# Optimization experiments

Measured on AMD Instinct MI355X. Metric: run time of the kernel, lower is better.

## Reference

```python
import jax, jax.numpy as jnp
import numpy as np

B, K, N, M = 32, 128, 128, 256  # batch, num_classes(==n_dim), n_dim, samples-per-matrix
EPSILON = 0.1
LAMBDA_SOFTMAX = 0.1
LEARNING_RATE = 0.01
BN_EPS = 1e-5


def setup_inputs() -> dict:
    key = jax.random.key(0)
    k1, k2, k3 = jax.random.split(key, 3)
    x = jax.random.normal(k1, (B, N, M), dtype=jnp.float32)
    A = jax.random.normal(k2, (K, N, N), dtype=jnp.float32) * 0.1
    EC_proto = jnp.einsum('kij,klj->kil', A, A)  # per-class PSD prototype covariances (K,N,N)
    EC_count = jax.random.uniform(k3, (K,), dtype=jnp.float32, minval=1.0, maxval=100.0)
    return {"x": x, "EC_proto": EC_proto, "EC_count": EC_count}


def reference(x, EC_proto, EC_count):
    n = x.shape[1]
    dtype = x.dtype
    # BatchNorm1d(num_classes, affine=False, track_running_stats=False): batch stats over (N, L)
    mean = x.mean(axis=(0, 2), keepdims=True)
    var = x.var(axis=(0, 2), keepdims=True)  # biased variance, as torch uses for normalization
    x = (x - mean) / jnp.sqrt(var + BN_EPS)

    eye = jnp.eye(n, dtype=dtype)
    total = EC_count.sum()
    has_counts = total > 1e-6

    # E branch: global expansion operator
    e_alpha = jnp.where(has_counts, n / (EPSILON * EPSILON * total), jnp.zeros((), dtype))
    e = e_alpha * jnp.linalg.inv(e_alpha * EC_proto.sum(0) + eye)  # (N,N)
    e_x_z = jnp.einsum('ij,bjm->bim', e, x)  # (B,N,M)

    # C branch: per-class compression operators
    bool_depth = (EC_count != 0).astype(dtype)  # (K,)
    count_fix = EC_count + (1.0 - bool_depth)
    c_alpha = (n / (count_fix * EPSILON * EPSILON) * bool_depth)[:, None, None]  # (K,1,1)
    c = c_alpha * jnp.linalg.inv(c_alpha * EC_proto + eye[None])  # (K,N,N)
    c_x_z = jnp.einsum('kij,bjm->bkim', c, x)  # (B,K,N,M)

    # Frobenius norm per (b,k), rescaled to sum to 10 over classes
    norm = jnp.sqrt((c_x_z * c_x_z).sum(axis=(2, 3)))  # (B,K)
    norm = 10.0 * norm / norm.sum(axis=1, keepdims=True)

    pi = jax.nn.softmax(-LAMBDA_SOFTMAX * norm, axis=1) * bool_depth  # (B,K)
    gama = jnp.where(has_counts, EC_count / total, jnp.zeros_like(EC_count))  # (K,)

    z_d = e_x_z - jnp.einsum('k,bkim,bk->bim', gama, c_x_z, pi)  # (B,N,M)
    return x + LEARNING_RATE * z_d
```

## Files before the change

### kernel.cpp

```cpp
#include <hip/hip_runtime.h>
#include <math.h>

#define Bb 32
#define Kk 128
#define Nn 128
#define Mm 256
#define EPS2 0.01f
#define LAMBDA_S 0.1f
#define LR 0.01f
#define BN_EPS_C 1e-5f

#define SWZ(c) (((c) & 14) | (((c) & 1) << 4) | (((c) >> 4) & 1))

__device__ __forceinline__ float readlane_f(float v, int lane) {
  return __int_as_float(__builtin_amdgcn_readlane(__float_as_int(v), lane));
}

__global__ void kPre(const float* __restrict__ P, float* __restrict__ Psum) {
  int e = blockIdx.x * 256 + threadIdx.x;
  float s = 0.f;
  #pragma unroll 8
  for (int k = 0; k < Kk; ++k) s += P[(size_t)k * 16384 + e];
  Psum[e] = s;
}

__global__ __launch_bounds__(512, 1) void kIR(
    const float* __restrict__ P, const float* __restrict__ Psum,
    const float* __restrict__ cnt, float* __restrict__ C,
    const float* __restrict__ x, float* __restrict__ R,
    float* __restrict__ rbuf, float* __restrict__ meanB,
    float* __restrict__ rstdB) {
  __shared__ __align__(16) float LB[8448];
  int bx = blockIdx.x;
  int t = threadIdx.x;

  if (bx < 129) {
    float* Mt = LB;
    float* Rb = LB + 2112;
    float* redc = LB + 4160;
    int mat = bx;
    int tx = t & 15;
    int wy = t >> 4;

    float cv = cnt[t & 127];
    float sr = cv;
    #pragma unroll
    for (int o = 32; o > 0; o >>= 1) sr += __shfl_down(sr, o, 64);
    if ((t & 63) == 0) redc[t >> 6] = sr;
    __syncthreads();
    float total = redc[0] + redc[1];
    bool has = total > 1e-6f;
    float av;
    if (mat < 128) {
      float c = cnt[mat];
      float bk = (c != 0.0f) ? 1.0f : 0.0f;
      float cfix = c + (1.0f - bk);
      av = (float)Nn / (cfix * EPS2) * bk;
    } else {
      av = has ? ((float)Nn / (EPS2 * total)) : 0.0f;
    }
    const float* src = (mat < 128) ? (P + (size_t)mat * 16384) : Psum;

    float a[4][8];
    #pragma unroll
    for (int i = 0; i < 4; ++i) {
      int row = wy * 4 + i;
      float4 p0 = *(const float4*)&src[row * 128 + tx * 8];
      float4 p1 = *(const float4*)&src[row * 128 + tx * 8 + 4];
      a[i][0] = av * p0.x; a[i][1] = av * p0.y; a[i][2] = av * p0.z; a[i][3] = av * p0.w;
      a[i][4] = av * p1.x; a[i][5] = av * p1.y; a[i][6] = av * p1.z; a[i][7] = av * p1.w;
      if (tx == (wy >> 1)) a[i][(wy & 1) * 4 + i] += 1.0f;
    }

    for (int kb = 0; kb < 8; ++kb) {
      int k0 = kb * 16;
      if ((wy >> 2) == kb) {
        int d = wy & 3;
        #pragma unroll
        for (int i = 0; i < 4; ++i) {
          *(float4*)&Rb[(d * 4 + i) * 128 + SWZ(2 * tx) * 4] =
              make_float4(a[i][0], a[i][1], a[i][2], a[i][3]);
          *(float4*)&Rb[(d * 4 + i) * 128 + SWZ(2 * tx + 1) * 4] =
              make_float4(a[i][4], a[i][5], a[i][6], a[i][7]);
        }
      }
      if ((tx >> 1) == kb) {
        int dh = tx & 1;
        #pragma unroll
        for (int i = 0; i < 4; ++i)
          #pragma unroll
          for (int j = 0; j < 8; ++j)
            Mt[(dh * 8 + j) * 132 + wy * 4 + i] = a[i][j];
      }
      __syncthreads();

      if (t < 64) {
        int l = t;
        float m[2][16];
        #pragma unroll
        for (int d = 0; d < 2; ++d)
          #pragma unroll
          for (int j = 0; j < 16; ++j)
            m[d][j] = Mt[j * 132 + 2 * l + d];
        #pragma unroll
        for (int q = 0; q < 16; ++q) {
          int lq = (k0 + q) >> 1;
          float pr[16];
          #pragma unroll
          for (int j = 0; j < 16; ++j) pr[j] = readlane_f(m[q & 1][j], lq);
          float piv = pr[q];
          float r0 = __builtin_amdgcn_rcpf(piv);
          float pinv = r0 * (2.0f - piv * r0);
          #pragma unroll
          for (int d = 0; d < 2; ++d) {
            float f = m[d][q];
            bool isp = (2 * l + d == k0 + q);
            float g = isp ? (1.0f - pinv) : f * pinv;
            #pragma unroll
            for (int j = 0; j < 16; ++j) m[d][j] = fmaf(-g, pr[j], m[d][j]);
            m[d][q] = isp ? pinv : -g;
          }
        }
        #pragma unroll
        for (int d = 0; d < 2; ++d)
          #pragma unroll
          for (int j = 0; j < 16; ++j)
            Mt[j * 132 + 2 * l + d] = m[d][j];
      }
      __syncthreads();

      if ((wy >> 2) == kb) {
        #pragma unroll
        for (int i = 0; i < 4; ++i)
          #pragma unroll
          for (int j = 0; j < 8; ++j) a[i][j] = 0.0f;
      }
      #pragma unroll
      for (int q = 0; q < 16; ++q) {
        float4 m0 = *(const float4*)&Mt[q * 132 + wy * 4];
        float4 r0 = *(const float4*)&Rb[q * 128 + SWZ(2 * tx) * 4];
        float4 r1 = *(const float4*)&Rb[q * 128 + SWZ(2 * tx + 1) * 4];
        float mq[4] = {m0.x, m0.y, m0.z, m0.w};
        float rq[8] = {r0.x, r0.y, r0.z, r0.w, r1.x, r1.y, r1.z, r1.w};
        #pragma unroll
        for (int i = 0; i < 4; ++i)
          #pragma unroll
          for (int j = 0; j < 8; ++j)
            a[i][j] = fmaf(mq[i], rq[j], a[i][j]);
      }
      if ((tx >> 1) == kb) {
        int dh = tx & 1;
        #pragma unroll
        for (int j = 0; j < 8; ++j) {
          float4 v0 = *(const float4*)&Mt[(dh * 8 + j) * 132 + wy * 4];
          a[0][j] = v0.x; a[1][j] = v0.y; a[2][j] = v0.z; a[3][j] = v0.w;
        }
      }
      __syncthreads();
    }

    float* dst = C + (size_t)mat * 16384;
    #pragma unroll
    for (int i = 0; i < 4; ++i) {
      int row = wy * 4 + i;
      float4 v0 = make_float4(av * a[i][0], av * a[i][1], av * a[i][2], av * a[i][3]);
      float4 v1 = make_float4(av * a[i][4], av * a[i][5], av * a[i][6], av * a[i][7]);
      *(float4*)&dst[row * 128 + tx * 8] = v0;
      *(float4*)&dst[row * 128 + tx * 8 + 4] = v1;
    }
  } else if (bx < 193) {
    int bxx = bx - 129;
    int b = bxx >> 1;
    int jbase = (bxx & 1) * 64;
    float* X = LB;
    int tx = t & 15, wy = t >> 4;
    float acc[4][4] = {};
    float rsum = 0.f;
    for (int mc = 0; mc < Mm; mc += 64) {
      __syncthreads();
      #pragma unroll
      for (int c = 0; c < 16; ++c) {
        int e = c * 512 + t;
        int i = e >> 6, mm = e & 63;
        X[i * 65 + mm] = x[(size_t)b * (Nn * Mm) + i * Mm + mc + mm];
      }
      __syncthreads();
      if (t < 128) {
        #pragma unroll
        for (int mm = 0; mm < 64; ++mm) rsum += X[t * 65 + mm];
      }
      for (int mm = 0; mm < 64; ++mm) {
        float ai[4], bj[4];
        #pragma unroll
        for (int q = 0; q < 4; ++q) ai[q] = X[(wy * 4 + q) * 65 + mm];
        #pragma unroll
        for (int q = 0; q < 4; ++q) bj[q] = X[(jbase + tx * 4 + q) * 65 + mm];
        #pragma unroll
        for (int qi = 0; qi < 4; ++qi)
          #pragma unroll
          for (int qj = 0; qj < 4; ++qj)
            acc[qi][qj] = fmaf(ai[qi], bj[qj], acc[qi][qj]);
      }
    }
    float* dst = R + (size_t)b * 16384;
    #pragma unroll
    for (int qi = 0; qi < 4; ++qi) {
      float4 v = make_float4(acc[qi][0], acc[qi][1], acc[qi][2], acc[qi][3]);
      *(float4*)&dst[(wy * 4 + qi) * 128 + jbase + tx * 4] = v;
    }
    if (jbase == 0 && t < 128) rbuf[b * 128 + t] = rsum;
  } else {
    int n = bx - 193;
    int m = t & 255, bh = t >> 8;
    float s = 0.f, s2 = 0.f;
    #pragma unroll
    for (int q = 0; q < 16; ++q) {
      float v = x[(size_t)(bh * 16 + q) * (Nn * Mm) + n * Mm + m];
      s += v; s2 += v * v;
    }
    #pragma unroll
    for (int o = 32; o > 0; o >>= 1) {
      s += __shfl_down(s, o, 64);
      s2 += __shfl_down(s2, o, 64);
    }
    if ((t & 63) == 0) { LB[t >> 6] = s; LB[16 + (t >> 6)] = s2; }
    __syncthreads();
    if (t == 0) {
      float S = 0.f, S2 = 0.f;
      #pragma unroll
      for (int w = 0; w < 8; ++w) { S += LB[w]; S2 += LB[16 + w]; }
      float mean = S * (1.0f / (Bb * Mm));
      float var = S2 * (1.0f / (Bb * Mm)) - mean * mean;
      meanB[n] = mean;
      rstdB[n] = 1.0f / sqrtf(var + BN_EPS_C);
    }
  }
}

__global__ __launch_bounds__(256, 1) void kGN(const float* __restrict__ C,
                                              const float* __restrict__ R,
                                              const float* __restrict__ rbuf,
                                              const float* __restrict__ meanB,
                                              const float* __restrict__ rstdB,
                                              float* __restrict__ norm2h) {
  __shared__ __align__(16) float LB[128 * 128];
  __shared__ float redb[4][32];
  __shared__ float muL[128], rsL[128], uL[128];
  int k = blockIdx.x >> 2, qh = blockIdx.x & 3;
  int t = threadIdx.x;
  if (t < 128) { muL[t] = meanB[t]; rsL[t] = rstdB[t]; }
  const float* src = C + (size_t)k * 16384;
  for (int c = 0; c < 64; ++c) LB[c * 256 + t] = src[c * 256 + t];
  __syncthreads();
  int tx = t & 15, ty = t >> 4;
  int i0 = ty * 8, j0 = qh * 32 + tx * 2;
  float acc[8][2] = {};
  #pragma unroll 2
  for (int l = 0; l < 128; ++l) {
    float ai[8];
    *(float4*)&ai[0] = *(const float4*)&LB[l * 128 + i0];
    *(float4*)&ai[4] = *(const float4*)&LB[l * 128 + i0 + 4];
    float2 bj = *(const float2*)&LB[l * 128 + j0];
    #pragma unroll
    for (int qi = 0; qi < 8; ++qi) {
      acc[qi][0] = fmaf(ai[qi], bj.x, acc[qi][0]);
      acc[qi][1] = fmaf(ai[qi], bj.y, acc[qi][1]);
    }
  }
  __syncthreads();
  float sj0 = rsL[j0], sj1 = rsL[j0 + 1];
  #pragma unroll
  for (int qi = 0; qi < 8; ++qi) {
    float si = rsL[i0 + qi];
    *(float2*)&LB[(i0 + qi) * 32 + tx * 2] =
        make_float2(acc[qi][0] * si * sj0, acc[qi][1] * si * sj1);
  }
  __syncthreads();
  if (t < 128) {
    float u = 0.f;
    #pragma unroll
    for (int jl = 0; jl < 32; ++jl)
      u = fmaf(LB[t * 32 + jl], muL[qh * 32 + jl], u);
    uL[t] = u;
  }
  float nacc[32];
  #pragma unroll
  for (int b = 0; b < 32; ++b) nacc[b] = 0.0f;
  #pragma unroll
  for (int q = 0; q < 4; ++q) {
    int el = (q * 256 + t) * 4;
    float4 g = *(const float4*)&LB[el];
    int i = el >> 5, jl = el & 31;
    const float* sb = R + i * 128 + qh * 32 + jl;
    #pragma unroll
    for (int b = 0; b < 32; ++b) {
      float4 sv = *(const float4*)&sb[(size_t)b * 16384];
      nacc[b] = fmaf(g.x, sv.x, nacc[b]);
      nacc[b] = fmaf(g.y, sv.y, nacc[b]);
      nacc[b] = fmaf(g.z, sv.z, nacc[b]);
      nacc[b] = fmaf(g.w, sv.w, nacc[b]);
    }
  }
  #pragma unroll
  for (int b = 0; b < 32; ++b) {
    float v = nacc[b];
    #pragma unroll
    for (int o = 32; o > 0; o >>= 1) v += __shfl_down(v, o, 64);
    nacc[b] = v;
  }
  if ((t & 63) == 0) {
    int w = t >> 6;
    #pragma unroll
    for (int b = 0; b < 32; ++b) redb[w][b] = nacc[b];
  }
  __syncthreads();
  if (t < 32) {
    float corr = 0.f;
    for (int i = 0; i < 128; ++i)
      corr = fmaf(uL[i], 256.0f * muL[i] - 2.0f * rbuf[t * 128 + i], corr);
    norm2h[(size_t)k * 128 + qh * 32 + t] =
        redb[0][t] + redb[1][t] + redb[2][t] + redb[3][t] + corr;
  }
}

__global__ void k7n(const float* __restrict__ norm2h, const float* __restrict__ cnt,
                    float* __restrict__ wT) {
  int b = blockIdx.x;
  int k = threadIdx.x;
  const float* nh = norm2h + (size_t)k * 128 + b;
  float n2 = nh[0] + nh[32] + nh[64] + nh[96];
  float norm = sqrtf(fmaxf(n2, 0.0f));
  float cv = cnt[k];
  __shared__ float r1[2], r2[2], r3[2];
  float tt = cv, r = norm;
  #pragma unroll
  for (int o = 32; o > 0; o >>= 1) {
    tt += __shfl_down(tt, o, 64);
    r += __shfl_down(r, o, 64);
  }
  if ((k & 63) == 0) { r1[k >> 6] = tt; r2[k >> 6] = r; }
  __syncthreads();
  float total = r1[0] + r1[1];
  float sumn = r2[0] + r2[1];
  float nr = 10.0f * norm / fmaxf(sumn, 1e-30f);
  float ex = expf(-LAMBDA_S * nr);
  float e2 = ex;
  #pragma unroll
  for (int o = 32; o > 0; o >>= 1) e2 += __shfl_down(e2, o, 64);
  if ((k & 63) == 0) r3[k >> 6] = e2;
  __syncthreads();
  float sume = r3[0] + r3[1];
  float bk = (cv != 0.0f) ? 1.0f : 0.0f;
  float pi = (ex / sume) * bk;
  float gama = (total > 1e-6f) ? (cv / total) : 0.0f;
  wT[k * 32 + b] = gama * pi;
}

__global__ __launch_bounds__(256, 1) void k8_k(const float* __restrict__ C,
                                               const float* __restrict__ E,
                                               const float* __restrict__ wT,
                                               float* __restrict__ F) {
  int e = blockIdx.x * 256 + threadIdx.x;
  int b0 = blockIdx.y * 8;
  float acc[8];
  float ev = E[e];
  #pragma unroll
  for (int b = 0; b < 8; ++b) acc[b] = ev;
  #pragma unroll 4
  for (int k = 0; k < 128; ++k) {
    float cv = C[(size_t)k * 16384 + e];
    const float* wk = wT + k * 32 + b0;
    #pragma unroll
    for (int b = 0; b < 8; ++b) acc[b] = fmaf(-wk[b], cv, acc[b]);
  }
  #pragma unroll
  for (int b = 0; b < 8; ++b) F[(size_t)(b0 + b) * 16384 + e] = acc[b];
}

__global__ __launch_bounds__(256, 1) void k9_k(const float* __restrict__ F,
                                               const float* __restrict__ x,
                                               const float* __restrict__ meanB,
                                               const float* __restrict__ rstdB,
                                               float* __restrict__ out) {
  int bx = blockIdx.x;
  int b = bx >> 3, y = bx & 7;
  int mq = y >> 1, ih = y & 1;
  __shared__ __align__(16) float Ft[64 * 68];
  __shared__ __align__(16) float Xt[64 * 68];
  __shared__ float muL[128], rsL[128];
  int t = threadIdx.x;
  if (t < 128) { muL[t] = meanB[t]; rsL[t] = rstdB[t]; }
  int tx = t & 15, ty = t >> 4;
  float acc[4][4] = {};
  for (int jc = 0; jc < 128; jc += 64) {
    __syncthreads();
    #pragma unroll
    for (int q = 0; q < 4; ++q) {
      int e = q * 256 + t;
      int i = e >> 4, j4 = e & 15;
      *(float4*)&Ft[i * 68 + j4 * 4] =
          *(const float4*)&F[(size_t)b * 16384 + (ih * 64 + i) * 128 + jc + j4 * 4];
    }
    #pragma unroll
    for (int q = 0; q < 4; ++q) {
      int e = q * 256 + t;
      int jj = e >> 4, m4 = e & 15;
      float4 g = *(const float4*)&x[(size_t)b * (Nn * Mm) + (jc + jj) * Mm + mq * 64 + m4 * 4];
      float mu = muL[jc + jj], rs = rsL[jc + jj];
      *(float4*)&Xt[jj * 68 + m4 * 4] =
          make_float4((g.x - mu) * rs, (g.y - mu) * rs, (g.z - mu) * rs, (g.w - mu) * rs);
    }
    __syncthreads();
    for (int j4 = 0; j4 < 16; ++j4) {
      float4 fi[4], xm[4];
      #pragma unroll
      for (int r = 0; r < 4; ++r)
        fi[r] = *(const float4*)&Ft[(ty * 4 + r) * 68 + j4 * 4];
      #pragma unroll
      for (int r = 0; r < 4; ++r)
        xm[r] = *(const float4*)&Xt[(j4 * 4 + r) * 68 + tx * 4];
      #pragma unroll
      for (int qi = 0; qi < 4; ++qi) {
        #pragma unroll
        for (int qm = 0; qm < 4; ++qm) {
          float xv = ((const float*)&xm[0])[qm];
          acc[qi][qm] = fmaf(fi[qi].x, xv, acc[qi][qm]);
          xv = ((const float*)&xm[1])[qm];
          acc[qi][qm] = fmaf(fi[qi].y, xv, acc[qi][qm]);
          xv = ((const float*)&xm[2])[qm];
          acc[qi][qm] = fmaf(fi[qi].z, xv, acc[qi][qm]);
          xv = ((const float*)&xm[3])[qm];
          acc[qi][qm] = fmaf(fi[qi].w, xv, acc[qi][qm]);
        }
      }
    }
  }
  int i0 = ih * 64 + ty * 4, m0 = mq * 64 + tx * 4;
  #pragma unroll
  for (int qi = 0; qi < 4; ++qi) {
    float4 xv = *(const float4*)&x[(size_t)b * (Nn * Mm) + (i0 + qi) * Mm + m0];
    float mu = muL[i0 + qi], rs = rsL[i0 + qi];
    float4 o;
    o.x = fmaf(LR, acc[qi][0], (xv.x - mu) * rs);
    o.y = fmaf(LR, acc[qi][1], (xv.y - mu) * rs);
    o.z = fmaf(LR, acc[qi][2], (xv.z - mu) * rs);
    o.w = fmaf(LR, acc[qi][3], (xv.w - mu) * rs);
    *(float4*)&out[(size_t)b * (Nn * Mm) + (i0 + qi) * Mm + m0] = o;
  }
}

extern "C" void kernel_launch(void* const* d_in, const int* in_sizes, int n_in,
                              void* d_out, int out_size, void* d_ws, size_t ws_size,
                              hipStream_t stream) {
  const float* x = (const float*)d_in[0];
  const float* P = (const float*)d_in[1];
  const float* cnt = (const float*)d_in[2];
  float* out = (float*)d_out;

  float* ws = (float*)d_ws;
  float* C = ws;
  float* R = C + 2113536;
  float* norm2h = R + 524288;
  float* wT = norm2h + 16384;
  float* F = wT + 4096;
  float* Psum = F + 524288;
  float* rbuf = Psum + 16384;
  float* meanB = rbuf + 4096;
  float* rstdB = meanB + 128;
  size_t need_bytes = (size_t)((rstdB + 128) - ws) * sizeof(float);
  if (ws_size < need_bytes) return;

  hipLaunchKernelGGL(kPre, dim3(64), dim3(256), 0, stream, P, Psum);
  hipLaunchKernelGGL(kIR, dim3(321), dim3(512), 0, stream, P, Psum, cnt, C, x, R,
                     rbuf, meanB, rstdB);
  hipLaunchKernelGGL(kGN, dim3(512), dim3(256), 0, stream, C, R, rbuf, meanB,
                     rstdB, norm2h);
  hipLaunchKernelGGL(k7n, dim3(32), dim3(128), 0, stream, norm2h, cnt, wT);
  hipLaunchKernelGGL(k8_k, dim3(64, 4), dim3(256), 0, stream, C,
                     C + (size_t)128 * 16384, wT, F);
  hipLaunchKernelGGL(k9_k, dim3(256), dim3(256), 0, stream, F, x, meanB, rstdB, out);
}
```

Baseline: 162.5 us.

## Fuse all six kernels into one cooperative persistent kernel with grid syncs

```diff
diff --git a/kernel.cpp b/kernel.cpp
--- a/kernel.cpp
+++ b/kernel.cpp
@@ -1,5 +1,8 @@
 #include <hip/hip_runtime.h>
+#include <hip/hip_cooperative_groups.h>
 #include <math.h>
+
+namespace cg = cooperative_groups;
 
 #define Bb 32
 #define Kk 128
@@ -16,28 +19,98 @@
   return __int_as_float(__builtin_amdgcn_readlane(__float_as_int(v), lane));
 }
 
-__global__ void kPre(const float* __restrict__ P, float* __restrict__ Psum) {
-  int e = blockIdx.x * 256 + threadIdx.x;
-  float s = 0.f;
-  #pragma unroll 8
-  for (int k = 0; k < Kk; ++k) s += P[(size_t)k * 16384 + e];
-  Psum[e] = s;
-}
-
-__global__ __launch_bounds__(512, 1) void kIR(
-    const float* __restrict__ P, const float* __restrict__ Psum,
-    const float* __restrict__ cnt, float* __restrict__ C,
-    const float* __restrict__ x, float* __restrict__ R,
-    float* __restrict__ rbuf, float* __restrict__ meanB,
-    float* __restrict__ rstdB) {
-  __shared__ __align__(16) float LB[8448];
+__global__ __launch_bounds__(512, 1) void mega(
+    const float* __restrict__ x, const float* __restrict__ P,
+    const float* __restrict__ cnt, float* __restrict__ C, float* __restrict__ R,
+    float* __restrict__ Psum, float* __restrict__ norm2h, float* __restrict__ wT,
+    float* __restrict__ F, float* __restrict__ rbuf, float* __restrict__ meanB,
+    float* __restrict__ rstdB, float* __restrict__ out) {
+  cg::grid_group gg = cg::this_grid();
+  __shared__ __align__(16) float LB[16384];
+  __shared__ float redb[8][32];
+  __shared__ float muL[128], rsL[128], uL[128];
+  __shared__ float redc[8];
   int bx = blockIdx.x;
   int t = threadIdx.x;
+
+  if (bx < 128) {
+    int n = bx, m = t & 255, bh = t >> 8;
+    float s = 0.f, s2 = 0.f;
+    #pragma unroll
+    for (int q = 0; q < 16; ++q) {
+      float v = x[(size_t)(bh * 16 + q) * (Nn * Mm) + n * Mm + m];
+      s += v; s2 += v * v;
+    }
+    #pragma unroll
+    for (int o = 32; o > 0; o >>= 1) {
+      s += __shfl_down(s, o, 64);
+      s2 += __shfl_down(s2, o, 64);
+    }
+    if ((t & 63) == 0) { redb[0][t >> 6] = s; redb[1][t >> 6] = s2; }
+    __syncthreads();
+    if (t == 0) {
+      float S = 0.f, S2 = 0.f;
+      #pragma unroll
+      for (int w = 0; w < 8; ++w) { S += redb[0][w]; S2 += redb[1][w]; }
+      float mean = S * (1.0f / (Bb * Mm));
+      float var = S2 * (1.0f / (Bb * Mm)) - mean * mean;
+      meanB[n] = mean;
+      rstdB[n] = 1.0f / sqrtf(var + BN_EPS_C);
+    }
+  } else if (bx < 192) {
+    int bxx = bx - 128;
+    int b = bxx >> 1;
+    int jbase = (bxx & 1) * 64;
+    float* X = LB;
+    int tx = t & 15, wy = t >> 4;
+    float acc[4][4] = {};
+    float rsum = 0.f;
+    for (int mc = 0; mc < Mm; mc += 64) {
+      __syncthreads();
+      #pragma unroll
+      for (int c = 0; c < 16; ++c) {
+        int e = c * 512 + t;
+        int i = e >> 6, mm = e & 63;
+        X[i * 65 + mm] = x[(size_t)b * (Nn * Mm) + i * Mm + mc + mm];
+      }
+      __syncthreads();
+      if (t < 128) {
+        #pragma unroll
+        for (int mm = 0; mm < 64; ++mm) rsum += X[t * 65 + mm];
+      }
+      for (int mm = 0; mm < 64; ++mm) {
+        float ai[4], bj[4];
+        #pragma unroll
+        for (int q = 0; q < 4; ++q) ai[q] = X[(wy * 4 + q) * 65 + mm];
+        #pragma unroll
+        for (int q = 0; q < 4; ++q) bj[q] = X[(jbase + tx * 4 + q) * 65 + mm];
+        #pragma unroll
+        for (int qi = 0; qi < 4; ++qi)
+          #pragma unroll
+          for (int qj = 0; qj < 4; ++qj)
+            acc[qi][qj] = fmaf(ai[qi], bj[qj], acc[qi][qj]);
+      }
+    }
+    float* dst = R + (size_t)b * 16384;
+    #pragma unroll
+    for (int qi = 0; qi < 4; ++qi) {
+      float4 v = make_float4(acc[qi][0], acc[qi][1], acc[qi][2], acc[qi][3]);
+      *(float4*)&dst[(wy * 4 + qi) * 128 + jbase + tx * 4] = v;
+    }
+    if (jbase == 0 && t < 128) rbuf[b * 128 + t] = rsum;
+  } else if (bx < 224) {
+    int e = (bx - 192) * 512 + t;
+    float s = 0.f;
+    #pragma unroll 8
+    for (int k = 0; k < Kk; ++k) s += P[(size_t)k * 16384 + e];
+    Psum[e] = s;
+  }
+  __threadfence();
+  gg.sync();
 
   if (bx < 129) {
     float* Mt = LB;
     float* Rb = LB + 2112;
-    float* redc = LB + 4160;
     int mat = bx;
     int tx = t & 15;
     int wy = t >> 4;
@@ -168,284 +241,217 @@
       *(float4*)&dst[row * 128 + tx * 8] = v0;
       *(float4*)&dst[row * 128 + tx * 8 + 4] = v1;
     }
-  } else if (bx < 193) {
-    int bxx = bx - 129;
-    int b = bxx >> 1;
-    int jbase = (bxx & 1) * 64;
-    float* X = LB;
-    int tx = t & 15, wy = t >> 4;
+  }
+  __threadfence();
+  gg.sync();
+
+  {
+    int k = bx >> 1, h = bx & 1;
+    if (t < 128) { muL[t] = meanB[t]; rsL[t] = rstdB[t]; }
+    const float* src = C + (size_t)k * 16384;
+    #pragma unroll
+    for (int c = 0; c < 32; ++c) LB[c * 512 + t] = src[c * 512 + t];
+    __syncthreads();
+    int tx = t & 15, ty = t >> 4;
+    int i0 = ty * 4, j0 = h * 64 + tx * 4;
     float acc[4][4] = {};
-    float rsum = 0.f;
-    for (int mc = 0; mc < Mm; mc += 64) {
-      __syncthreads();
-      #pragma unroll
-      for (int c = 0; c < 16; ++c) {
-        int e = c * 512 + t;
-        int i = e >> 6, mm = e & 63;
-        X[i * 65 + mm] = x[(size_t)b * (Nn * Mm) + i * Mm + mc + mm];
-      }
-      __syncthreads();
-      if (t < 128) {
-        #pragma unroll
-        for (int mm = 0; mm < 64; ++mm) rsum += X[t * 65 + mm];
-      }
-      for (int mm = 0; mm < 64; ++mm) {
-        float ai[4], bj[4];
-        #pragma unroll
-        for (int q = 0; q < 4; ++q) ai[q] = X[(wy * 4 + q) * 65 + mm];
-        #pragma unroll
-        for (int q = 0; q < 4; ++q) bj[q] = X[(jbase + tx * 4 + q) * 65 + mm];
-        #pragma unroll
-        for (int qi = 0; qi < 4; ++qi)
-          #pragma unroll
-          for (int qj = 0; qj < 4; ++qj)
-            acc[qi][qj] = fmaf(ai[qi], bj[qj], acc[qi][qj]);
-      }
-    }
-    float* dst = R + (size_t)b * 16384;
+    #pragma unroll 2
+    for (int l = 0; l < 128; ++l) {
+      float ai[4], bj[4];
+      *(float4*)&ai[0] = *(const float4*)&LB[l * 128 + i0];
+      *(float4*)&bj[0] = *(const float4*)&LB[l * 128 + j0];
+      #pragma unroll
+      for (int qi = 0; qi < 4; ++qi)
+        #pragma unroll
+        for (int qj = 0; qj < 4; ++qj)
+          acc[qi][qj] = fmaf(ai[qi], bj[qj], acc[qi][qj]);
+    }
+    __syncthreads();
+    float sj[4] = {rsL[j0], rsL[j0 + 1], rsL[j0 + 2], rsL[j0 + 3]};
     #pragma unroll
     for (int qi = 0; qi < 4; ++qi) {
-      float4 v = make_float4(acc[qi][0], acc[qi][1], acc[qi][2], acc[qi][3]);
-      *(float4*)&dst[(wy * 4 + qi) * 128 + jbase + tx * 4] = v;
-    }
-    if (jbase == 0 && t < 128) rbuf[b * 128 + t] = rsum;
-  } else {
-    int n = bx - 193;
-    int m = t & 255, bh = t >> 8;
-    float s = 0.f, s2 = 0.f;
-    #pragma unroll
-    for (int q = 0; q < 16; ++q) {
-      float v = x[(size_t)(bh * 16 + q) * (Nn * Mm) + n * Mm + m];
-      s += v; s2 += v * v;
-    }
+      float si = rsL[i0 + qi];
+      *(float4*)&LB[(i0 + qi) * 64 + tx * 4] =
+          make_float4(acc[qi][0] * si * sj[0], acc[qi][1] * si * sj[1],
+                      acc[qi][2] * si * sj[2], acc[qi][3] * si * sj[3]);
+    }
+    __syncthreads();
+    if (t < 128) {
+      float u = 0.f;
+      #pragma unroll
+      for (int jl = 0; jl < 64; ++jl)
+        u = fmaf(LB[t * 64 + jl], muL[h * 64 + jl], u);
+      uL[t] = u;
+    }
+    float nacc[32];
+    #pragma unroll
+    for (int b = 0; b < 32; ++b) nacc[b] = 0.0f;
+    #pragma unroll
+    for (int q = 0; q < 4; ++q) {
+      int idx = q * 512 + t;
+      int el = idx * 4;
+      float4 g = *(const float4*)&LB[el];
+      int i = el >> 6, jl = el & 63;
+      const float* sb = R + i * 128 + h * 64 + jl;
+      #pragma unroll
+      for (int b = 0; b < 32; ++b) {
+        float4 sv = *(const float4*)&sb[(size_t)b * 16384];
+        nacc[b] = fmaf(g.x, sv.x, nacc[b]);
+        nacc[b] = fmaf(g.y, sv.y, nacc[b]);
+        nacc[b] = fmaf(g.z, sv.z, nacc[b]);
+        nacc[b] = fmaf(g.w, sv.w, nacc[b]);
+      }
+    }
+    #pragma unroll
+    for (int b = 0; b < 32; ++b) {
+      float v = nacc[b];
+      #pragma unroll
+      for (int o = 32; o > 0; o >>= 1) v += __shfl_down(v, o, 64);
+      nacc[b] = v;
+    }
+    if ((t & 63) == 0) {
+      int w = t >> 6;
+      #pragma unroll
+      for (int b = 0; b < 32; ++b) redb[w][b] = nacc[b];
+    }
+    __syncthreads();
+    if (t < 32) {
+      float s = 0.f;
+      #pragma unroll
+      for (int w = 0; w < 8; ++w) s += redb[w][t];
+      float corr = 0.f;
+      for (int i = 0; i < 128; ++i)
+        corr = fmaf(uL[i], 256.0f * muL[i] - 2.0f * rbuf[t * 128 + i], corr);
+      norm2h[(size_t)k * 64 + h * 32 + t] = s + corr;
+    }
+  }
+  __threadfence();
+  gg.sync();
+
+  if (bx < 32) {
+    int b2 = bx;
+    float cv2 = 0.f, nrm = 0.f, ex = 0.f;
+    if (t < 128) {
+      float n2 = norm2h[(size_t)t * 64 + b2] + norm2h[(size_t)t * 64 + 32 + b2];
+      nrm = sqrtf(fmaxf(n2, 0.0f));
+      cv2 = cnt[t];
+    }
+    float tt = cv2, rr = nrm;
     #pragma unroll
     for (int o = 32; o > 0; o >>= 1) {
-      s += __shfl_down(s, o, 64);
-      s2 += __shfl_down(s2, o, 64);
-    }
-    if ((t & 63) == 0) { LB[t >> 6] = s; LB[16 + (t >> 6)] = s2; }
-    __syncthreads();
-    if (t == 0) {
-      float S = 0.f, S2 = 0.f;
-      #pragma unroll
-      for (int w = 0; w < 8; ++w) { S += LB[w]; S2 += LB[16 + w]; }
-      float mean = S * (1.0f / (Bb * Mm));
-      float var = S2 * (1.0f / (Bb * Mm)) - mean * mean;
-      meanB[n] = mean;
-      rstdB[n] = 1.0f / sqrtf(var + BN_EPS_C);
-    }
-  }
-}
-
-__global__ __launch_bounds__(256, 1) void kGN(const float* __restrict__ C,
-                                              const float* __restrict__ R,
-                                              const float* __restrict__ rbuf,
-                                              const float* __restrict__ meanB,
-                                              const float* __restrict__ rstdB,
-                                              float* __restrict__ norm2h) {
-  __shared__ __align__(16) float LB[128 * 128];
-  __shared__ float redb[4][32];
-  __shared__ float muL[128], rsL[128], uL[128];
-  int k = blockIdx.x >> 2, qh = blockIdx.x & 3;
-  int t = threadIdx.x;
-  if (t < 128) { muL[t] = meanB[t]; rsL[t] = rstdB[t]; }
-  const float* src = C + (size_t)k * 16384;
-  for (int c = 0; c < 64; ++c) LB[c * 256 + t] = src[c * 256 + t];
-  __syncthreads();
-  int tx = t & 15, ty = t >> 4;
-  int i0 = ty * 8, j0 = qh * 32 + tx * 2;
-  float acc[8][2] = {};
-  #pragma unroll 2
-  for (int l = 0; l < 128; ++l) {
-    float ai[8];
-    *(float4*)&ai[0] = *(const float4*)&LB[l * 128 + i0];
-    *(float4*)&ai[4] = *(const float4*)&LB[l * 128 + i0 + 4];
-    float2 bj = *(const float2*)&LB[l * 128 + j0];
-    #pragma unroll
-    for (int qi = 0; qi < 8; ++qi) {
-      acc[qi][0] = fmaf(ai[qi], bj.x, acc[qi][0]);
-      acc[qi][1] = fmaf(ai[qi], bj.y, acc[qi][1]);
-    }
-  }
-  __syncthreads();
-  float sj0 = rsL[j0], sj1 = rsL[j0 + 1];
-  #pragma unroll
-  for (int qi = 0; qi < 8; ++qi) {
-    float si = rsL[i0 + qi];
-    *(float2*)&LB[(i0 + qi) * 32 + tx * 2] =
-        make_float2(acc[qi][0] * si * sj0, acc[qi][1] * si * sj1);
-  }
-  __syncthreads();
-  if (t < 128) {
-    float u = 0.f;
-    #pragma unroll
-    for (int jl = 0; jl < 32; ++jl)
-      u = fmaf(LB[t * 32 + jl], muL[qh * 32 + jl], u);
-    uL[t] = u;
-  }
-  float nacc[32];
-  #pragma unroll
-  for (int b = 0; b < 32; ++b) nacc[b] = 0.0f;
-  #pragma unroll
-  for (int q = 0; q < 4; ++q) {
-    int el = (q * 256 + t) * 4;
-    float4 g = *(const float4*)&LB[el];
-    int i = el >> 5, jl = el & 31;
-    const float* sb = R + i * 128 + qh * 32 + jl;
-    #pragma unroll
-    for (int b = 0; b < 32; ++b) {
-      float4 sv = *(const float4*)&sb[(size_t)b * 16384];
-      nacc[b] = fmaf(g.x, sv.x, nacc[b]);
-      nacc[b] = fmaf(g.y, sv.y, nacc[b]);
-      nacc[b] = fmaf(g.z, sv.z, nacc[b]);
-      nacc[b] = fmaf(g.w, sv.w, nacc[b]);
-    }
-  }
-  #pragma unroll
-  for (int b = 0; b < 32; ++b) {
-    float v = nacc[b];
-    #pragma unroll
-    for (int o = 32; o > 0; o >>= 1) v += __shfl_down(v, o, 64);
-    nacc[b] = v;
-  }
-  if ((t & 63) == 0) {
-    int w = t >> 6;
-    #pragma unroll
-    for (int b = 0; b < 32; ++b) redb[w][b] = nacc[b];
-  }
-  __syncthreads();
-  if (t < 32) {
-    float corr = 0.f;
-    for (int i = 0; i < 128; ++i)
-      corr = fmaf(uL[i], 256.0f * muL[i] - 2.0f * rbuf[t * 128 + i], corr);
-    norm2h[(size_t)k * 128 + qh * 32 + t] =
-        redb[0][t] + redb[1][t] + redb[2][t] + redb[3][t] + corr;
-  }
-}
-
-__global__ void k7n(const float* __restrict__ norm2h, const float* __restrict__ cnt,
-                    float* __restrict__ wT) {
-  int b = blockIdx.x;
-  int k = threadIdx.x;
-  const float* nh = norm2h + (size_t)k * 128 + b;
-  float n2 = nh[0] + nh[32] + nh[64] + nh[96];
-  float norm = sqrtf(fmaxf(n2, 0.0f));
-  float cv = cnt[k];
-  __shared__ float r1[2], r2[2], r3[2];
-  float tt = cv, r = norm;
-  #pragma unroll
-  for (int o = 32; o > 0; o >>= 1) {
-    tt += __shfl_down(tt, o, 64);
-    r += __shfl_down(r, o, 64);
-  }
-  if ((k & 63) == 0) { r1[k >> 6] = tt; r2[k >> 6] = r; }
-  __syncthreads();
-  float total = r1[0] + r1[1];
-  float sumn = r2[0] + r2[1];
-  float nr = 10.0f * norm / fmaxf(sumn, 1e-30f);
-  float ex = expf(-LAMBDA_S * nr);
-  float e2 = ex;
-  #pragma unroll
-  for (int o = 32; o > 0; o >>= 1) e2 += __shfl_down(e2, o, 64);
-  if ((k & 63) == 0) r3[k >> 6] = e2;
-  __syncthreads();
-  float sume = r3[0] + r3[1];
-  float bk = (cv != 0.0f) ? 1.0f : 0.0f;
-  float pi = (ex / sume) * bk;
-  float gama = (total > 1e-6f) ? (cv / total) : 0.0f;
-  wT[k * 32 + b] = gama * pi;
-}
-
-__global__ __launch_bounds__(256, 1) void k8_k(const float* __restrict__ C,
-                                               const float* __restrict__ E,
-                                               const float* __restrict__ wT,
-                                               float* __restrict__ F) {
-  int e = blockIdx.x * 256 + threadIdx.x;
-  int b0 = blockIdx.y * 8;
-  float acc[8];
-  float ev = E[e];
-  #pragma unroll
-  for (int b = 0; b < 8; ++b) acc[b] = ev;
-  #pragma unroll 4
-  for (int k = 0; k < 128; ++k) {
-    float cv = C[(size_t)k * 16384 + e];
-    const float* wk = wT + k * 32 + b0;
-    #pragma unroll
-    for (int b = 0; b < 8; ++b) acc[b] = fmaf(-wk[b], cv, acc[b]);
-  }
-  #pragma unroll
-  for (int b = 0; b < 8; ++b) F[(size_t)(b0 + b) * 16384 + e] = acc[b];
-}
-
-__global__ __launch_bounds__(256, 1) void k9_k(const float* __restrict__ F,
-                                               const float* __restrict__ x,
-                                               const float* __restrict__ meanB,
-                                               const float* __restrict__ rstdB,
-                                               float* __restrict__ out) {
-  int bx = blockIdx.x;
-  int b = bx >> 3, y = bx & 7;
-  int mq = y >> 1, ih = y & 1;
-  __shared__ __align__(16) float Ft[64 * 68];
-  __shared__ __align__(16) float Xt[64 * 68];
-  __shared__ float muL[128], rsL[128];
-  int t = threadIdx.x;
-  if (t < 128) { muL[t] = meanB[t]; rsL[t] = rstdB[t]; }
-  int tx = t & 15, ty = t >> 4;
-  float acc[4][4] = {};
-  for (int jc = 0; jc < 128; jc += 64) {
-    __syncthreads();
-    #pragma unroll
-    for (int q = 0; q < 4; ++q) {
-      int e = q * 256 + t;
-      int i = e >> 4, j4 = e & 15;
-      *(float4*)&Ft[i * 68 + j4 * 4] =
-          *(const float4*)&F[(size_t)b * 16384 + (ih * 64 + i) * 128 + jc + j4 * 4];
-    }
-    #pragma unroll
-    for (int q = 0; q < 4; ++q) {
-      int e = q * 256 + t;
-      int jj = e >> 4, m4 = e & 15;
-      float4 g = *(const float4*)&x[(size_t)b * (Nn * Mm) + (jc + jj) * Mm + mq * 64 + m4 * 4];
-      float mu = muL[jc + jj], rs = rsL[jc + jj];
-      *(float4*)&Xt[jj * 68 + m4 * 4] =
-          make_float4((g.x - mu) * rs, (g.y - mu) * rs, (g.z - mu) * rs, (g.w - mu) * rs);
-    }
-    __syncthreads();
-    for (int j4 = 0; j4 < 16; ++j4) {
-      float4 fi[4], xm[4];
-      #pragma unroll
-      for (int r = 0; r < 4; ++r)
-        fi[r] = *(const float4*)&Ft[(ty * 4 + r) * 68 + j4 * 4];
-      #pragma unroll
-      for (int r = 0; r < 4; ++r)
-        xm[r] = *(const float4*)&Xt[(j4 * 4 + r) * 68 + tx * 4];
-      #pragma unroll
-      for (int qi = 0; qi < 4; ++qi) {
-        #pragma unroll
-        for (int qm = 0; qm < 4; ++qm) {
-          float xv = ((const float*)&xm[0])[qm];
-          acc[qi][qm] = fmaf(fi[qi].x, xv, acc[qi][qm]);
-          xv = ((const float*)&xm[1])[qm];
-          acc[qi][qm] = fmaf(fi[qi].y, xv, acc[qi][qm]);
-          xv = ((const float*)&xm[2])[qm];
-          acc[qi][qm] = fmaf(fi[qi].z, xv, acc[qi][qm]);
-          xv = ((const float*)&xm[3])[qm];
-          acc[qi][qm] = fmaf(fi[qi].w, xv, acc[qi][qm]);
+      tt += __shfl_down(tt, o, 64);
+      rr += __shfl_down(rr, o, 64);
+    }
+    if ((t & 63) == 0) { redc[t >> 6] = tt; uL[t >> 6] = rr; }
+    __syncthreads();
+    float total = redc[0] + redc[1];
+    float sumn = uL[0] + uL[1];
+    if (t < 128) {
+      float nr = 10.0f * nrm / fmaxf(sumn, 1e-30f);
+      ex = expf(-LAMBDA_S * nr);
+    }
+    float e2 = ex;
+    #pragma unroll
+    for (int o = 32; o > 0; o >>= 1) e2 += __shfl_down(e2, o, 64);
+    if ((t & 63) == 0) uL[8 + (t >> 6)] = e2;
+    __syncthreads();
+    float sume = uL[8] + uL[9];
+    if (t < 128) {
+      float bk = (cv2 != 0.0f) ? 1.0f : 0.0f;
+      float pi = (ex / sume) * bk;
+      float gama = (total > 1e-6f) ? (cv2 / total) : 0.0f;
+      wT[t * 32 + b2] = gama * pi;
+    }
+  }
+  __threadfence();
+  gg.sync();
+
+  {
+    int ec = bx & 31, by = bx >> 5;
+    if (by < 4) {
+      int e = ec * 512 + t;
+      int b0 = by * 8;
+      const float* E = C + (size_t)128 * 16384;
+      float acc[8];
+      float ev = E[e];
+      #pragma unroll
+      for (int b = 0; b < 8; ++b) acc[b] = ev;
+      #pragma unroll 4
+      for (int k = 0; k < 128; ++k) {
+        float cval = C[(size_t)k * 16384 + e];
+        const float* wk = wT + k * 32 + b0;
+        #pragma unroll
+        for (int b = 0; b < 8; ++b) acc[b] = fmaf(-wk[b], cval, acc[b]);
+      }
+      #pragma unroll
+      for (int b = 0; b < 8; ++b) F[(size_t)(b0 + b) * 16384 + e] = acc[b];
+    }
+  }
+  __threadfence();
+  gg.sync();
+
+  {
+    int b = bx >> 3, y = bx & 7;
+    int mq = y >> 1, ih = y & 1;
+    float* Ft = LB;
+    float* Xt = LB + 4352;
+    int tx = t & 15, ty = t >> 4;
+    float acc[2][4] = {};
+    for (int jc = 0; jc < 128; jc += 64) {
+      __syncthreads();
+      #pragma unroll
+      for (int q = 0; q < 2; ++q) {
+        int e = q * 512 + t;
+        int i = e >> 4, j4 = e & 15;
+        *(float4*)&Ft[i * 68 + j4 * 4] =
+            *(const float4*)&F[(size_t)b * 16384 + (ih * 64 + i) * 128 + jc + j4 * 4];
+      }
+      #pragma unroll
+      for (int q = 0; q < 2; ++q) {
+        int e = q * 512 + t;
+        int jj = e >> 4, m4 = e & 15;
+        float4 g = *(const float4*)&x[(size_t)b * (Nn * Mm) + (jc + jj) * Mm + mq * 64 + m4 * 4];
+        float mu = muL[jc + jj], rs = rsL[jc + jj];
+        *(float4*)&Xt[jj * 68 + m4 * 4] =
+            make_float4((g.x - mu) * rs, (g.y - mu) * rs, (g.z - mu) * rs, (g.w - mu) * rs);
+      }
+      __syncthreads();
+      for (int j4 = 0; j4 < 16; ++j4) {
+        float4 fi[2], xm[4];
+        #pragma unroll
+        for (int r = 0; r < 2; ++r)
+          fi[r] = *(const float4*)&Ft[(ty * 2 + r) * 68 + j4 * 4];
+        #pragma unroll
+        for (int r = 0; r < 4; ++r)
+          xm[r] = *(const float4*)&Xt[(j4 * 4 + r) * 68 + tx * 4];
+        #pragma unroll
+        for (int qi = 0; qi < 2; ++qi) {
+          #pragma unroll
+          for (int qm = 0; qm < 4; ++qm) {
+            float xv = ((const float*)&xm[0])[qm];
+            acc[qi][qm] = fmaf(fi[qi].x, xv, acc[qi][qm]);
+            xv = ((const float*)&xm[1])[qm];
+            acc[qi][qm] = fmaf(fi[qi].y, xv, acc[qi][qm]);
+            xv = ((const float*)&xm[2])[qm];
+            acc[qi][qm] = fmaf(fi[qi].z, xv, acc[qi][qm]);
+            xv = ((const float*)&xm[3])[qm];
+            acc[qi][qm] = fmaf(fi[qi].w, xv, acc[qi][qm]);
+          }
         }
       }
     }
-  }
-  int i0 = ih * 64 + ty * 4, m0 = mq * 64 + tx * 4;
-  #pragma unroll
-  for (int qi = 0; qi < 4; ++qi) {
-    float4 xv = *(const float4*)&x[(size_t)b * (Nn * Mm) + (i0 + qi) * Mm + m0];
-    float mu = muL[i0 + qi], rs = rsL[i0 + qi];
-    float4 o;
-    o.x = fmaf(LR, acc[qi][0], (xv.x - mu) * rs);
-    o.y = fmaf(LR, acc[qi][1], (xv.y - mu) * rs);
-    o.z = fmaf(LR, acc[qi][2], (xv.z - mu) * rs);
-    o.w = fmaf(LR, acc[qi][3], (xv.w - mu) * rs);
-    *(float4*)&out[(size_t)b * (Nn * Mm) + (i0 + qi) * Mm + m0] = o;
+    int i0 = ih * 64 + ty * 2, m0 = mq * 64 + tx * 4;
+    #pragma unroll
+    for (int qi = 0; qi < 2; ++qi) {
+      float4 xv = *(const float4*)&x[(size_t)b * (Nn * Mm) + (i0 + qi) * Mm + m0];
+      float mu = muL[i0 + qi], rs = rsL[i0 + qi];
+      float4 o;
+      o.x = fmaf(LR, acc[qi][0], (xv.x - mu) * rs);
+      o.y = fmaf(LR, acc[qi][1], (xv.y - mu) * rs);
+      o.z = fmaf(LR, acc[qi][2], (xv.z - mu) * rs);
+      o.w = fmaf(LR, acc[qi][3], (xv.w - mu) * rs);
+      *(float4*)&out[(size_t)b * (Nn * Mm) + (i0 + qi) * Mm + m0] = o;
+    }
   }
 }
 
@@ -460,23 +466,20 @@
   float* ws = (float*)d_ws;
   float* C = ws;
   float* R = C + 2113536;
-  float* norm2h = R + 524288;
-  float* wT = norm2h + 16384;
-  float* F = wT + 4096;
+  float* F = R + 524288;
   float* Psum = F + 524288;
-  float* rbuf = Psum + 16384;
+  float* norm2h = Psum + 16384;
+  float* wT = norm2h + 8192;
+  float* rbuf = wT + 4096;
   float* meanB = rbuf + 4096;
   float* rstdB = meanB + 128;
   size_t need_bytes = (size_t)((rstdB + 128) - ws) * sizeof(float);
   if (ws_size < need_bytes) return;
 
-  hipLaunchKernelGGL(kPre, dim3(64), dim3(256), 0, stream, P, Psum);
-  hipLaunchKernelGGL(kIR, dim3(321), dim3(512), 0, stream, P, Psum, cnt, C, x, R,
-                     rbuf, meanB, rstdB);
-  hipLaunchKernelGGL(kGN, dim3(512), dim3(256), 0, stream, C, R, rbuf, meanB,
-                     rstdB, norm2h);
-  hipLaunchKernelGGL(k7n, dim3(32), dim3(128), 0, stream, norm2h, cnt, wT);
-  hipLaunchKernelGGL(k8_k, dim3(64, 4), dim3(256), 0, stream, C,
-                     C + (size_t)128 * 16384, wT, F);
-  hipLaunchKernelGGL(k9_k, dim3(256), dim3(256), 0, stream, F, x, meanB, rstdB, out);
+  void* args[] = {(void*)&x,      (void*)&P,    (void*)&cnt,   (void*)&C,
+                  (void*)&R,      (void*)&Psum, (void*)&norm2h,(void*)&wT,
+                  (void*)&F,      (void*)&rbuf, (void*)&meanB, (void*)&rstdB,
+                  (void*)&out};
+  hipLaunchCooperativeKernel((const void*)mega, dim3(256), dim3(512), args, 0,
+                             stream);
 }
```

New measurement: 519.8 us. 3.2x slower.

## Fuse prototype-sum into inversion kernel and shrink blocks to 256 threads

Applied to the files above, without the earlier changes.

```diff
diff --git a/kernel.cpp b/kernel.cpp
--- a/kernel.cpp
+++ b/kernel.cpp
@@ -16,20 +16,11 @@
   return __int_as_float(__builtin_amdgcn_readlane(__float_as_int(v), lane));
 }
 
-__global__ void kPre(const float* __restrict__ P, float* __restrict__ Psum) {
-  int e = blockIdx.x * 256 + threadIdx.x;
-  float s = 0.f;
-  #pragma unroll 8
-  for (int k = 0; k < Kk; ++k) s += P[(size_t)k * 16384 + e];
-  Psum[e] = s;
-}
-
-__global__ __launch_bounds__(512, 1) void kIR(
-    const float* __restrict__ P, const float* __restrict__ Psum,
-    const float* __restrict__ cnt, float* __restrict__ C,
-    const float* __restrict__ x, float* __restrict__ R,
-    float* __restrict__ rbuf, float* __restrict__ meanB,
-    float* __restrict__ rstdB) {
+__global__ __launch_bounds__(256, 4) void kBig(
+    const float* __restrict__ P, const float* __restrict__ cnt,
+    float* __restrict__ C, const float* __restrict__ x, float* __restrict__ R,
+    float* __restrict__ rbuf, float* __restrict__ meanB, float* __restrict__ rstdB,
+    float* __restrict__ Psum) {
   __shared__ __align__(16) float LB[8448];
   int bx = blockIdx.x;
   int t = threadIdx.x;
@@ -39,8 +30,7 @@
     float* Rb = LB + 2112;
     float* redc = LB + 4160;
     int mat = bx;
-    int tx = t & 15;
-    int wy = t >> 4;
+    int tx = t & 15, ty = t >> 4;
 
     float cv = cnt[t & 127];
     float sr = cv;
@@ -59,38 +49,61 @@
     } else {
       av = has ? ((float)Nn / (EPS2 * total)) : 0.0f;
     }
-    const float* src = (mat < 128) ? (P + (size_t)mat * 16384) : Psum;
-
-    float a[4][8];
-    #pragma unroll
-    for (int i = 0; i < 4; ++i) {
-      int row = wy * 4 + i;
-      float4 p0 = *(const float4*)&src[row * 128 + tx * 8];
-      float4 p1 = *(const float4*)&src[row * 128 + tx * 8 + 4];
-      a[i][0] = av * p0.x; a[i][1] = av * p0.y; a[i][2] = av * p0.z; a[i][3] = av * p0.w;
-      a[i][4] = av * p1.x; a[i][5] = av * p1.y; a[i][6] = av * p1.z; a[i][7] = av * p1.w;
-      if (tx == (wy >> 1)) a[i][(wy & 1) * 4 + i] += 1.0f;
+    float a[8][8];
+    if (mat < 128) {
+      const float* src = P + (size_t)mat * 16384;
+      #pragma unroll
+      for (int i = 0; i < 8; ++i) {
+        int row = ty * 8 + i;
+        float4 p0 = *(const float4*)&src[row * 128 + tx * 8];
+        float4 p1 = *(const float4*)&src[row * 128 + tx * 8 + 4];
+        a[i][0] = av * p0.x; a[i][1] = av * p0.y; a[i][2] = av * p0.z; a[i][3] = av * p0.w;
+        a[i][4] = av * p1.x; a[i][5] = av * p1.y; a[i][6] = av * p1.z; a[i][7] = av * p1.w;
+        if (tx == ty) a[i][i] += 1.0f;
+      }
+    } else {
+      #pragma unroll
+      for (int i = 0; i < 8; ++i)
+        #pragma unroll
+        for (int j = 0; j < 8; ++j) a[i][j] = 0.0f;
+      for (int k = 0; k < Kk; ++k) {
+        const float* src = P + (size_t)k * 16384;
+        #pragma unroll
+        for (int i = 0; i < 8; ++i) {
+          int row = ty * 8 + i;
+          float4 p0 = *(const float4*)&src[row * 128 + tx * 8];
+          float4 p1 = *(const float4*)&src[row * 128 + tx * 8 + 4];
+          a[i][0] += p0.x; a[i][1] += p0.y; a[i][2] += p0.z; a[i][3] += p0.w;
+          a[i][4] += p1.x; a[i][5] += p1.y; a[i][6] += p1.z; a[i][7] += p1.w;
+        }
+      }
+      #pragma unroll
+      for (int i = 0; i < 8; ++i) {
+        #pragma unroll
+        for (int j = 0; j < 8; ++j) a[i][j] *= av;
+        if (tx == ty) a[i][i] += 1.0f;
+      }
     }
 
     for (int kb = 0; kb < 8; ++kb) {
       int k0 = kb * 16;
-      if ((wy >> 2) == kb) {
-        int d = wy & 3;
-        #pragma unroll
-        for (int i = 0; i < 4; ++i) {
-          *(float4*)&Rb[(d * 4 + i) * 128 + SWZ(2 * tx) * 4] =
+      if ((ty >> 1) == kb) {
+        int d = ty & 1;
+        #pragma unroll
+        for (int i = 0; i < 8; ++i) {
+          *(float4*)&Rb[(d * 8 + i) * 128 + SWZ(2 * tx) * 4] =
               make_float4(a[i][0], a[i][1], a[i][2], a[i][3]);
-          *(float4*)&Rb[(d * 4 + i) * 128 + SWZ(2 * tx + 1) * 4] =
+          *(float4*)&Rb[(d * 8 + i) * 128 + SWZ(2 * tx + 1) * 4] =
               make_float4(a[i][4], a[i][5], a[i][6], a[i][7]);
         }
       }
       if ((tx >> 1) == kb) {
         int dh = tx & 1;
         #pragma unroll
-        for (int i = 0; i < 4; ++i)
+        for (int i = 0; i < 8; ++i)
           #pragma unroll
           for (int j = 0; j < 8; ++j)
-            Mt[(dh * 8 + j) * 132 + wy * 4 + i] = a[i][j];
+            Mt[(dh * 8 + j) * 132 + ty * 8 + i] = a[i][j];
       }
       __syncthreads();
 
@@ -129,21 +142,22 @@
       }
       __syncthreads();
 
-      if ((wy >> 2) == kb) {
-        #pragma unroll
-        for (int i = 0; i < 4; ++i)
+      if ((ty >> 1) == kb) {
+        #pragma unroll
+        for (int i = 0; i < 8; ++i)
           #pragma unroll
           for (int j = 0; j < 8; ++j) a[i][j] = 0.0f;
       }
       #pragma unroll
       for (int q = 0; q < 16; ++q) {
-        float4 m0 = *(const float4*)&Mt[q * 132 + wy * 4];
+        float4 m0 = *(const float4*)&Mt[q * 132 + ty * 8];
+        float4 m1 = *(const float4*)&Mt[q * 132 + ty * 8 + 4];
         float4 r0 = *(const float4*)&Rb[q * 128 + SWZ(2 * tx) * 4];
         float4 r1 = *(const float4*)&Rb[q * 128 + SWZ(2 * tx + 1) * 4];
-        float mq[4] = {m0.x, m0.y, m0.z, m0.w};
+        float mq[8] = {m0.x, m0.y, m0.z, m0.w, m1.x, m1.y, m1.z, m1.w};
         float rq[8] = {r0.x, r0.y, r0.z, r0.w, r1.x, r1.y, r1.z, r1.w};
         #pragma unroll
-        for (int i = 0; i < 4; ++i)
+        for (int i = 0; i < 8; ++i)
           #pragma unroll
           for (int j = 0; j < 8; ++j)
             a[i][j] = fmaf(mq[i], rq[j], a[i][j]);
@@ -152,8 +166,10 @@
         int dh = tx & 1;
         #pragma unroll
         for (int j = 0; j < 8; ++j) {
-          float4 v0 = *(const float4*)&Mt[(dh * 8 + j) * 132 + wy * 4];
+          float4 v0 = *(const float4*)&Mt[(dh * 8 + j) * 132 + ty * 8];
+          float4 v1 = *(const float4*)&Mt[(dh * 8 + j) * 132 + ty * 8 + 4];
           a[0][j] = v0.x; a[1][j] = v0.y; a[2][j] = v0.z; a[3][j] = v0.w;
+          a[4][j] = v1.x; a[5][j] = v1.y; a[6][j] = v1.z; a[7][j] = v1.w;
         }
       }
       __syncthreads();
@@ -161,8 +177,8 @@
 
     float* dst = C + (size_t)mat * 16384;
     #pragma unroll
-    for (int i = 0; i < 4; ++i) {
-      int row = wy * 4 + i;
+    for (int i = 0; i < 8; ++i) {
+      int row = ty * 8 + i;
       float4 v0 = make_float4(av * a[i][0], av * a[i][1], av * a[i][2], av * a[i][3]);
       float4 v1 = make_float4(av * a[i][4], av * a[i][5], av * a[i][6], av * a[i][7]);
       *(float4*)&dst[row * 128 + tx * 8] = v0;
@@ -173,14 +189,13 @@
     int b = bxx >> 1;
     int jbase = (bxx & 1) * 64;
     float* X = LB;
-    int tx = t & 15, wy = t >> 4;
-    float acc[4][4] = {};
+    int tx = t & 15, ty = t >> 4;
+    float acc[8][4] = {};
     float rsum = 0.f;
     for (int mc = 0; mc < Mm; mc += 64) {
       __syncthreads();
-      #pragma unroll
-      for (int c = 0; c < 16; ++c) {
-        int e = c * 512 + t;
+      for (int c = 0; c < 32; ++c) {
+        int e = c * 256 + t;
         int i = e >> 6, mm = e & 63;
         X[i * 65 + mm] = x[(size_t)b * (Nn * Mm) + i * Mm + mc + mm];
       }
@@ -190,13 +205,13 @@
         for (int mm = 0; mm < 64; ++mm) rsum += X[t * 65 + mm];
       }
       for (int mm = 0; mm < 64; ++mm) {
-        float ai[4], bj[4];
-        #pragma unroll
-        for (int q = 0; q < 4; ++q) ai[q] = X[(wy * 4 + q) * 65 + mm];
+        float ai[8], bj[4];
+        #pragma unroll
+        for (int q = 0; q < 8; ++q) ai[q] = X[(ty * 8 + q) * 65 + mm];
         #pragma unroll
         for (int q = 0; q < 4; ++q) bj[q] = X[(jbase + tx * 4 + q) * 65 + mm];
         #pragma unroll
-        for (int qi = 0; qi < 4; ++qi)
+        for (int qi = 0; qi < 8; ++qi)
           #pragma unroll
           for (int qj = 0; qj < 4; ++qj)
             acc[qi][qj] = fmaf(ai[qi], bj[qj], acc[qi][qj]);
@@ -204,18 +219,17 @@
     }
     float* dst = R + (size_t)b * 16384;
     #pragma unroll
-    for (int qi = 0; qi < 4; ++qi) {
+    for (int qi = 0; qi < 8; ++qi) {
       float4 v = make_float4(acc[qi][0], acc[qi][1], acc[qi][2], acc[qi][3]);
-      *(float4*)&dst[(wy * 4 + qi) * 128 + jbase + tx * 4] = v;
+      *(float4*)&dst[(ty * 8 + qi) * 128 + jbase + tx * 4] = v;
     }
     if (jbase == 0 && t < 128) rbuf[b * 128 + t] = rsum;
-  } else {
+  } else if (bx < 321) {
     int n = bx - 193;
-    int m = t & 255, bh = t >> 8;
     float s = 0.f, s2 = 0.f;
     #pragma unroll
-    for (int q = 0; q < 16; ++q) {
-      float v = x[(size_t)(bh * 16 + q) * (Nn * Mm) + n * Mm + m];
+    for (int b = 0; b < Bb; ++b) {
+      float v = x[(size_t)b * (Nn * Mm) + n * Mm + t];
       s += v; s2 += v * v;
     }
     #pragma unroll
@@ -223,17 +237,22 @@
       s += __shfl_down(s, o, 64);
       s2 += __shfl_down(s2, o, 64);
     }
-    if ((t & 63) == 0) { LB[t >> 6] = s; LB[16 + (t >> 6)] = s2; }
+    if ((t & 63) == 0) { LB[t >> 6] = s; LB[8 + (t >> 6)] = s2; }
     __syncthreads();
     if (t == 0) {
-      float S = 0.f, S2 = 0.f;
-      #pragma unroll
-      for (int w = 0; w < 8; ++w) { S += LB[w]; S2 += LB[16 + w]; }
+      float S = LB[0] + LB[1] + LB[2] + LB[3];
+      float S2 = LB[8] + LB[9] + LB[10] + LB[11];
       float mean = S * (1.0f / (Bb * Mm));
       float var = S2 * (1.0f / (Bb * Mm)) - mean * mean;
       meanB[n] = mean;
       rstdB[n] = 1.0f / sqrtf(var + BN_EPS_C);
     }
+  } else {
+    int e = (bx - 321) * 256 + t;
+    float s = 0.f;
+    #pragma unroll 8
+    for (int k = 0; k < Kk; ++k) s += P[(size_t)k * 16384 + e];
+    Psum[e] = s;
   }
 }
 
@@ -470,9 +489,8 @@
   size_t need_bytes = (size_t)((rstdB + 128) - ws) * sizeof(float);
   if (ws_size < need_bytes) return;
 
-  hipLaunchKernelGGL(kPre, dim3(64), dim3(256), 0, stream, P, Psum);
-  hipLaunchKernelGGL(kIR, dim3(321), dim3(512), 0, stream, P, Psum, cnt, C, x, R,
-                     rbuf, meanB, rstdB);
+  hipLaunchKernelGGL(kBig, dim3(385), dim3(256), 0, stream, P, cnt, C, x, R,
+                     rbuf, meanB, rstdB, Psum);
   hipLaunchKernelGGL(kGN, dim3(512), dim3(256), 0, stream, C, R, rbuf, meanB,
                      rstdB, norm2h);
   hipLaunchKernelGGL(k7n, dim3(32), dim3(128), 0, stream, norm2h, cnt, wT);
```

Result: slower. 316.9 us (+95.0%).
